# Optimization experiments

Hardware: AMD Instinct MI355X
Metric: run time of the kernel (lower is better)

Reference implementation:

```python
import jax, jax.numpy as jnp
import numpy as np

# Module constants (from init_kwargs)
NB_IN = 4          # num_blocks_in
NB_OUT = 8         # num_blocks_out
BS_IN = 128        # block_size_in (hard-coded in source)
NHID = 4096
BS_OUT = NHID // NB_OUT   # 512, also att_out
TOPK = 4
DK = 64            # d_k = d_v, n_head = 1


def _group_linear(x, w):
    # x: (B, n_blocks, d_in), w: (n_blocks, d_in, d_out) -> (B, n_blocks, d_out)
    return jnp.einsum('bnd,nde->bne', x, w)


def _attend(q, k, v):
    # single-head scaled dot-product attention
    attn = jax.nn.softmax(jnp.einsum('bqd,bkd->bqk', q, k) / jnp.sqrt(jnp.asarray(DK, q.dtype)), axis=-1)
    return jnp.einsum('bqk,bkd->bqd', attn, v), attn


def setup_inputs() -> dict:
    key = jax.random.key(0)
    ks = jax.random.split(key, 20)
    s = 0.02
    d = {
        'inp': jax.random.normal(ks[0], (1024, NB_IN * BS_IN), jnp.float32),
        'hx': jax.random.normal(ks[1], (1024, NHID), jnp.float32),
        'cx': jax.random.normal(ks[2], (1024, NHID), jnp.float32),
        # inp_att (residual=False): GroupLinear q/k/v + fc
        'ia_wq': jax.random.normal(ks[3], (NB_OUT, BS_OUT, DK), jnp.float32) * s,
        'ia_wk': jax.random.normal(ks[4], (NB_IN + 1, BS_IN, DK), jnp.float32) * s,
        'ia_wv': jax.random.normal(ks[5], (NB_IN + 1, BS_IN, DK), jnp.float32) * s,
        'ia_fc_w': jax.random.normal(ks[6], (DK, BS_OUT), jnp.float32) * s,
        'ia_fc_b': jnp.zeros((BS_OUT,), jnp.float32),
        # mha (residual=True, gated)
        'mha_wq': jax.random.normal(ks[7], (NB_OUT, BS_OUT, DK), jnp.float32) * s,
        'mha_wk': jax.random.normal(ks[8], (NB_OUT, BS_OUT, DK), jnp.float32) * s,
        'mha_wv': jax.random.normal(ks[9], (NB_OUT, BS_OUT, DK), jnp.float32) * s,
        'mha_fc_w': jax.random.normal(ks[10], (DK, BS_OUT), jnp.float32) * s,
        'mha_fc_b': jnp.zeros((BS_OUT,), jnp.float32),
        'mha_gate_w': jax.random.normal(ks[11], (DK, BS_OUT), jnp.float32) * s,
        'mha_gate_b': jnp.zeros((BS_OUT,), jnp.float32),
        # block-diagonal LSTM (BlockLSTM after blockify_params): per-block LSTMCell
        'w_ih': jax.random.normal(ks[12], (NB_OUT, BS_OUT, 4 * BS_OUT), jnp.float32) * s,
        'w_hh': jax.random.normal(ks[13], (NB_OUT, BS_OUT, 4 * BS_OUT), jnp.float32) * s,
        'b_ih': jnp.zeros((NB_OUT, 4 * BS_OUT), jnp.float32),
        'b_hh': jnp.zeros((NB_OUT, 4 * BS_OUT), jnp.float32),
    }
    return d


def _forward(inp, hx, cx, ia_wq, ia_wk, ia_wv, ia_fc_w, ia_fc_b,
             mha_wq, mha_wk, mha_wv, mha_fc_w, mha_fc_b, mha_gate_w, mha_gate_b,
             w_ih, w_hh, b_ih, b_hh):
    B = inp.shape[0]
    # --- input attention (inp_att) ---
    x = inp.reshape(B, NB_IN, BS_IN)
    x = jnp.concatenate([x, jnp.zeros_like(x[:, :1])], axis=1)        # append null block -> (B, NB_IN+1, BS_IN)
    hb = hx.reshape(B, NB_OUT, BS_OUT)
    q = _group_linear(hb, ia_wq)                                      # (B, NB_OUT, DK)
    k = _group_linear(x, ia_wk)
    v = _group_linear(x, ia_wv)
    o, iatt = _attend(q, k, v)                                        # o:(B,NB_OUT,DK), iatt:(B,NB_OUT,NB_IN+1)
    inp_use = (o @ ia_fc_w + ia_fc_b).reshape(B, NB_OUT * BS_OUT)     # residual=False path

    # --- top-k block selection mask (detached) ---
    score = iatt[:, :, 0]                                             # (B, NB_OUT)
    thr = jax.lax.top_k(score, TOPK)[0][:, -1]                        # k-th largest per sample
    mask_blk = (score > thr[:, None] - 0.01).astype(hx.dtype)         # (B, NB_OUT)
    mask = jnp.broadcast_to(mask_blk[:, :, None], (B, NB_OUT, BS_OUT)).reshape(B, NHID)
    mask = jax.lax.stop_gradient(mask)

    # --- block-diagonal LSTM update ---
    xb = inp_use.reshape(B, NB_OUT, BS_OUT)
    cb = cx.reshape(B, NB_OUT, BS_OUT)
    gates = (jnp.einsum('bkd,kdg->bkg', xb, w_ih) + b_ih
             + jnp.einsum('bkd,kdg->bkg', hb, w_hh) + b_hh)           # (B, NB_OUT, 4*BS_OUT)
    i_g, f_g, g_g, o_g = jnp.split(gates, 4, axis=-1)
    c_new = jax.nn.sigmoid(f_g) * cb + jax.nn.sigmoid(i_g) * jnp.tanh(g_g)
    h_new = jax.nn.sigmoid(o_g) * jnp.tanh(c_new)                     # (B, NB_OUT, BS_OUT)
    cx_new = c_new.reshape(B, NHID)

    # --- inter-block attention (step_att, residual + gate) ---
    residual = h_new
    q2 = _group_linear(h_new, mha_wq)
    k2 = _group_linear(h_new, mha_wk)
    v2 = _group_linear(h_new, mha_wv)
    o2, _ = _attend(q2, k2, v2)                                       # (B, NB_OUT, DK)
    out = o2 @ mha_fc_w + mha_fc_b
    gate = jax.nn.sigmoid(o2 @ mha_gate_w + mha_gate_b)
    hx_new = (residual + gate * jnp.tanh(out)).reshape(B, NHID)

    # --- masked blend of old / new states ---
    hx_out = mask * hx_new + (1.0 - mask) * hx
    cx_out = mask * cx_new + (1.0 - mask) * cx
    return hx_out, cx_out, mask


def reference(inp, hx, cx, ia_wq, ia_wk, ia_wv, ia_fc_w, ia_fc_b,
              mha_wq, mha_wk, mha_wv, mha_fc_w, mha_fc_b, mha_gate_w, mha_gate_b,
              w_ih, w_hh, b_ih, b_hh):
    return _forward(inp, hx, cx, ia_wq, ia_wk, ia_wv, ia_fc_w, ia_fc_b,
                    mha_wq, mha_wk, mha_wv, mha_fc_w, mha_fc_b, mha_gate_w, mha_gate_b,
                    w_ih, w_hh, b_ih, b_hh)
```

## Files before the change

kernel.cpp:

```cpp
#include <hip/hip_runtime.h>
#include <hip/hip_bf16.h>

#define B_    1024
#define NHID_ 4096
#define NBO   8
#define BSO   512
#define DK_   64

typedef __bf16 bf16;
typedef __bf16 bf16x2 __attribute__((ext_vector_type(2)));
typedef __bf16 bf16x4 __attribute__((ext_vector_type(4)));
typedef __bf16 bf16x8 __attribute__((ext_vector_type(8)));
typedef float  f32x4  __attribute__((ext_vector_type(4)));

__device__ __forceinline__ float sigf(float x){
    float e = __expf(-x);
    return __builtin_amdgcn_rcpf(1.0f + e);
}
__device__ __forceinline__ float ftanh(float x){
    float e = __expf(2.0f*x);
    return 1.0f - 2.0f*__builtin_amdgcn_rcpf(e + 1.0f);
}

__device__ __forceinline__ void gload16(const void* g, void* lds){
    __builtin_amdgcn_global_load_lds((const __attribute__((address_space(1))) unsigned int*)g,
                                     (__attribute__((address_space(3))) unsigned int*)lds,
                                     16, 0, 0);
}

__global__ __launch_bounds__(256) void k_prep(
    const float* __restrict__ w_ih, const float* __restrict__ w_hh,
    const float* __restrict__ hx,
    const float* __restrict__ mha_wq, const float* __restrict__ mha_wk,
    const float* __restrict__ mha_wv, const float* __restrict__ ia_fc_w,
    const float* __restrict__ fc_w, const float* __restrict__ gate_w,
    bf16* __restrict__ wT, bf16* __restrict__ hb16, bf16* __restrict__ wqkvT,
    bf16* __restrict__ iafcT, bf16* __restrict__ fcgT)
{
    int bid = blockIdx.x;
    int t = threadIdx.x;
    if (bid < 4096){
        int c0 = (bid & 31)*64;
        int k0 = ((bid>>5)&7)*64;
        int z  = bid>>8;
        int n = z>>1, which = z&1;
        const float* src = (which ? w_hh : w_ih) + (size_t)n*512*2048;
        __shared__ float tile[64][65];
        #pragma unroll
        for (int it=0; it<4; ++it){
            int idx = t + it*256;
            int r = idx>>4, c4 = (idx&15)*4;
            *(float4*)&tile[r][c4] = *(const float4*)&src[(size_t)(k0+r)*2048 + c0 + c4];
        }
        __syncthreads();
        #pragma unroll
        for (int it=0; it<2; ++it){
            int idx = t + it*256;
            int c = idx>>3, r8 = (idx&7)*8;
            bf16x8 v;
            #pragma unroll
            for (int jj=0;jj<8;++jj) v[jj] = (bf16)tile[r8+jj][c];
            *(bf16x8*)&wT[((size_t)n*2048 + c0 + c)*1024 + which*512 + k0 + r8] = v;
        }
        return;
    }
    int gid = (bid-4096)*256 + t;
    if (gid < 1048576){
        float4 v = ((const float4*)hx)[gid];
        bf16x4 o; o.x=(bf16)v.x; o.y=(bf16)v.y; o.z=(bf16)v.z; o.w=(bf16)v.w;
        *(bf16x4*)&hb16[(size_t)gid*4] = o;
        return;
    }
    int e = gid - 1048576;
    if (e < 786432){
        int col = e >> 9, k = e & 511;
        int n = col / 192, c = col - n*192;
        int p = c >> 6, ee = c & 63;
        const float* s = (p==0) ? mha_wq : ((p==1) ? mha_wk : mha_wv);
        wqkvT[e] = (bf16)s[((size_t)n*512 + k)*64 + ee];
        return;
    }
    e -= 786432;
    if (e < 32768){
        int c = e>>6, k = e&63;
        iafcT[e] = (bf16)ia_fc_w[(size_t)k*512 + c];
        return;
    }
    e -= 32768;
    if (e < 65536){
        int cg = e>>6, k = e&63;
        int ct = cg>>6, j = cg&63;
        const float* s = (j<32) ? fc_w : gate_w;
        int col = ct*32 + (j&31);
        fcgT[e] = (bf16)s[(size_t)k*512 + col];
    }
}

__global__ __launch_bounds__(256) void k_qkv(const float* __restrict__ hx,
                                             const float* __restrict__ inp,
                                             const float* __restrict__ ia_wq,
                                             const float* __restrict__ ia_wk,
                                             const float* __restrict__ ia_wv,
                                             float* __restrict__ qbuf,
                                             float* __restrict__ kbuf,
                                             float* __restrict__ vbuf)
{
    int b0 = blockIdx.x*32, y = blockIdx.y, t = threadIdx.x;
    int tx = t&15, ty = t>>4;
    __shared__ float Af[32][36];
    __shared__ float W1[32][68];
    __shared__ float W2[32][68];
    if (y < 8){
        int n = y;
        float acc[2][4] = {};
        for (int k0=0; k0<512; k0+=32){
            { int row=t>>3, c4=(t&7)*4;
              *(float4*)&Af[row][c4] = *(const float4*)&hx[(size_t)(b0+row)*4096 + n*512 + k0 + c4]; }
            #pragma unroll
            for (int j=0;j<2;++j){
                int id = j*256 + t;
                int kk = id>>4, e4 = (id&15)*4;
                *(float4*)&W1[kk][e4] = *(const float4*)&ia_wq[(size_t)n*32768 + (size_t)(k0+kk)*64 + e4];
            }
            __syncthreads();
            #pragma unroll
            for (int kk4=0; kk4<8; ++kk4){
                float4 a0 = *(float4*)&Af[ty*2  ][kk4*4];
                float4 a1 = *(float4*)&Af[ty*2+1][kk4*4];
                #pragma unroll
                for (int j=0;j<4;++j){
                    float4 wv = *(float4*)&W1[kk4*4+j][tx*4];
                    float s0 = (j==0)?a0.x:((j==1)?a0.y:((j==2)?a0.z:a0.w));
                    float s1 = (j==0)?a1.x:((j==1)?a1.y:((j==2)?a1.z:a1.w));
                    acc[0][0]+=s0*wv.x; acc[0][1]+=s0*wv.y; acc[0][2]+=s0*wv.z; acc[0][3]+=s0*wv.w;
                    acc[1][0]+=s1*wv.x; acc[1][1]+=s1*wv.y; acc[1][2]+=s1*wv.z; acc[1][3]+=s1*wv.w;
                }
            }
            __syncthreads();
        }
        #pragma unroll
        for (int r=0;r<2;++r){
            float4 o; o.x=acc[r][0]; o.y=acc[r][1]; o.z=acc[r][2]; o.w=acc[r][3];
            *(float4*)&qbuf[(size_t)(b0+ty*2+r)*512 + n*64 + tx*4] = o;
        }
    } else {
        int jb = y-8;
        float ak[2][4] = {}, av[2][4] = {};
        for (int k0=0; k0<128; k0+=32){
            { int row=t>>3, c4=(t&7)*4;
              *(float4*)&Af[row][c4] = *(const float4*)&inp[(size_t)(b0+row)*512 + jb*128 + k0 + c4]; }
            #pragma unroll
            for (int j=0;j<2;++j){
                int id = j*256 + t;
                int kk = id>>4, e4 = (id&15)*4;
                *(float4*)&W1[kk][e4] = *(const float4*)&ia_wk[(size_t)jb*8192 + (size_t)(k0+kk)*64 + e4];
                *(float4*)&W2[kk][e4] = *(const float4*)&ia_wv[(size_t)jb*8192 + (size_t)(k0+kk)*64 + e4];
            }
            __syncthreads();
            #pragma unroll
            for (int kk4=0; kk4<8; ++kk4){
                float4 a0 = *(float4*)&Af[ty*2  ][kk4*4];
                float4 a1 = *(float4*)&Af[ty*2+1][kk4*4];
                #pragma unroll
                for (int j=0;j<4;++j){
                    float4 wk = *(float4*)&W1[kk4*4+j][tx*4];
                    float4 wv = *(float4*)&W2[kk4*4+j][tx*4];
                    float s0 = (j==0)?a0.x:((j==1)?a0.y:((j==2)?a0.z:a0.w));
                    float s1 = (j==0)?a1.x:((j==1)?a1.y:((j==2)?a1.z:a1.w));
                    ak[0][0]+=s0*wk.x; ak[0][1]+=s0*wk.y; ak[0][2]+=s0*wk.z; ak[0][3]+=s0*wk.w;
                    ak[1][0]+=s1*wk.x; ak[1][1]+=s1*wk.y; ak[1][2]+=s1*wk.z; ak[1][3]+=s1*wk.w;
                    av[0][0]+=s0*wv.x; av[0][1]+=s0*wv.y; av[0][2]+=s0*wv.z; av[0][3]+=s0*wv.w;
                    av[1][0]+=s1*wv.x; av[1][1]+=s1*wv.y; av[1][2]+=s1*wv.z; av[1][3]+=s1*wv.w;
                }
            }
            __syncthreads();
        }
        #pragma unroll
        for (int r=0;r<2;++r){
            float4 ok; ok.x=ak[r][0]; ok.y=ak[r][1]; ok.z=ak[r][2]; ok.w=ak[r][3];
            float4 ov; ov.x=av[r][0]; ov.y=av[r][1]; ov.z=av[r][2]; ov.w=av[r][3];
            *(float4*)&kbuf[(size_t)(b0+ty*2+r)*256 + jb*64 + tx*4] = ok;
            *(float4*)&vbuf[(size_t)(b0+ty*2+r)*256 + jb*64 + tx*4] = ov;
        }
    }
}

__global__ __launch_bounds__(256) void k_score(const float* __restrict__ qbuf,
                                               const float* __restrict__ kbuf,
                                               const float* __restrict__ vbuf,
                                               bf16* __restrict__ obuf,
                                               float* __restrict__ maskb,
                                               float* __restrict__ mask_out)
{
    int t = threadIdx.x, sb = t>>6, ts = t&63;
    int b = blockIdx.x*4 + sb;
    __shared__ float q_s[4][512];
    __shared__ float k_s[4][256];
    __shared__ float v_s[4][256];
    __shared__ float at_s[4][40];
    __shared__ float sc_s[4][8];
    __shared__ float mb_s[4][8];

    #pragma unroll
    for (int r=0;r<8;++r) q_s[sb][ts+r*64] = qbuf[(size_t)b*512 + ts + r*64];
    #pragma unroll
    for (int r=0;r<4;++r){
        k_s[sb][ts+r*64] = kbuf[(size_t)b*256 + ts + r*64];
        v_s[sb][ts+r*64] = vbuf[(size_t)b*256 + ts + r*64];
    }
    __syncthreads();
    if (ts < 40){
        int n = ts/5, j = ts%5;
        float s = 0.f;
        if (j < 4){
            const float* q = &q_s[sb][n*64];
            const float* k = &k_s[sb][j*64];
            for (int e=0;e<64;++e) s += q[e]*k[e];
            s *= 0.125f;
        }
        at_s[sb][ts] = s;
    }
    __syncthreads();
    if (ts < 8){
        float m = at_s[sb][ts*5];
        for (int j=1;j<5;++j) m = fmaxf(m, at_s[sb][ts*5+j]);
        float ex[5]; float sum=0.f;
        for (int j=0;j<5;++j){ ex[j]=__expf(at_s[sb][ts*5+j]-m); sum+=ex[j]; }
        float inv = 1.f/sum;
        for (int j=0;j<5;++j) at_s[sb][ts*5+j] = ex[j]*inv;
        sc_s[sb][ts] = ex[0]*inv;
    }
    __syncthreads();
    if (ts == 0){
        float s[8];
        for (int nn=0;nn<8;++nn) s[nn] = sc_s[sb][nn];
        for (int ii=1;ii<8;++ii){ float key=s[ii]; int jj=ii-1;
            while(jj>=0 && s[jj]<key){ s[jj+1]=s[jj]; --jj; } s[jj+1]=key; }
        float thr = s[3]-0.01f;
        for (int nn=0;nn<8;++nn) mb_s[sb][nn] = (sc_s[sb][nn] > thr) ? 1.0f : 0.0f;
    }
    __syncthreads();
    #pragma unroll
    for (int r=0;r<8;++r){
        int i = ts + r*64;
        int n = i>>6, e = i&63;
        float s = 0.f;
        #pragma unroll
        for (int j=0;j<4;++j) s += at_s[sb][n*5+j]*v_s[sb][j*64+e];
        obuf[(size_t)b*512 + i] = (bf16)s;
    }
    if (ts < 8) maskb[b*8+ts] = mb_s[sb][ts];
    float4* mo = (float4*)(mask_out + (size_t)b*4096);
    #pragma unroll
    for (int r=0;r<16;++r){
        int i4 = ts + r*64;
        float m = mb_s[sb][i4>>7];
        float4 mv; mv.x=m; mv.y=m; mv.z=m; mv.w=m;
        mo[i4] = mv;
    }
}

__global__ __launch_bounds__(256) void k_fc_ia(const bf16* __restrict__ obuf,
                                               const bf16* __restrict__ iafcT,
                                               const float* __restrict__ ia_fc_b,
                                               bf16* __restrict__ xb16)
{
    int bx = blockIdx.x, by = blockIdx.y;
    int t = threadIdx.x, w = t>>6, l = t&63, quad = l>>4, l16 = l&15;
    int wm = w&1, wd = w>>1;
    __shared__ bf16 A_s[64*72];
    __shared__ bf16 W_s[64*72];
    #pragma unroll
    for (int j=0;j<2;++j){
        int c = t + j*256;
        int row = c>>3, seg = c&7;
        *(bf16x8*)&A_s[row*72 + seg*8] = *(const bf16x8*)&obuf[((size_t)bx*64+row)*64 + seg*8];
        *(bf16x8*)&W_s[row*72 + seg*8] = *(const bf16x8*)&iafcT[((size_t)by*64+row)*64 + seg*8];
    }
    __syncthreads();
    f32x4 zero = {0.f,0.f,0.f,0.f};
    f32x4 acc[2][2] = {{zero,zero},{zero,zero}};
    #pragma unroll
    for (int k0=0;k0<64;k0+=32){
        bf16x8 a[2], bb[2];
        #pragma unroll
        for (int r=0;r<2;++r) a[r] = *(const bf16x8*)&A_s[(wm*32+r*16+l16)*72 + k0 + quad*8];
        #pragma unroll
        for (int c=0;c<2;++c) bb[c] = *(const bf16x8*)&W_s[(wd*32+c*16+l16)*72 + k0 + quad*8];
        #pragma unroll
        for (int r=0;r<2;++r)
            #pragma unroll
            for (int c=0;c<2;++c)
                acc[r][c] = __builtin_amdgcn_mfma_f32_16x16x32_bf16(a[r], bb[c], acc[r][c], 0,0,0);
    }
    #pragma unroll
    for (int c=0;c<2;++c){
        int col = by*64 + wd*32 + c*16 + l16;
        float bias = ia_fc_b[col];
        #pragma unroll
        for (int r=0;r<2;++r)
            #pragma unroll
            for (int v=0;v<4;++v){
                int row = bx*64 + wm*32 + r*16 + quad*4 + v;
                xb16[(size_t)row*512 + col] = (bf16)(acc[r][c][v] + bias);
            }
    }
}

__global__ __launch_bounds__(256,4) void k_lstm(
    const bf16* __restrict__ xb16, const bf16* __restrict__ hb16,
    const bf16* __restrict__ wT, const float* __restrict__ b_ih,
    const float* __restrict__ b_hh, const float* __restrict__ cx,
    const float* __restrict__ maskb,
    float* __restrict__ cx_out, bf16* __restrict__ hn16)
{
    int bid = blockIdx.x;
    int n = bid & 7;
    int i = bid >> 3;
    int d0 = (i & 15) * 32;
    int b0 = (i >> 4) * 128;
    int t = threadIdx.x;
    int w = t >> 6, l = t & 63;
    int quad = l >> 4, l16 = l & 15;
    int wm = w & 1, wd = w >> 1;

    __shared__ bf16 A_s[2][512*8];
    __shared__ bf16 W_s[2][512*8];

    f32x4 zero = {0.f,0.f,0.f,0.f};
    f32x4 acc[4][4];
    #pragma unroll
    for (int rf=0;rf<4;++rf)
        #pragma unroll
        for (int g=0;g<4;++g) acc[rf][g] = zero;

    const bf16* wbase = wT + (size_t)n*2048*1024;

    auto stage = [&](int buf, int k0){
        const bf16* ab = (k0 < 512) ? (xb16 + (size_t)n*512 + k0)
                                    : (hb16 + (size_t)n*512 + (k0-512));
        #pragma unroll
        for (int j=0;j<2;++j){
            int slot = j*256 + w*64 + l;
            int row = slot>>2, ss = slot&3;
            int seg = ss ^ ((row>>1)&3);
            gload16(ab + (size_t)(b0+row)*4096 + seg*8, &A_s[buf][(j*256 + w*64)*8]);
        }
        #pragma unroll
        for (int j=0;j<2;++j){
            int slot = j*256 + w*64 + l;
            int col = slot>>2, ss = slot&3;
            int seg = ss ^ ((col>>1)&3);
            int g = col>>5, dl = col&31;
            gload16(wbase + (size_t)(g*512 + d0 + dl)*1024 + k0 + seg*8,
                    &W_s[buf][(j*256 + w*64)*8]);
        }
    };

    stage(0, 0);
    for (int it = 0; it < 32; ++it){
        __syncthreads();
        if (it < 31) stage((it+1)&1, (it+1)*32);
        int buf = it & 1;
        bf16x8 a[4];
        #pragma unroll
        for (int rf=0;rf<4;++rf){
            int row = wm*64 + rf*16 + l16;
            int slot = row*4 + (quad ^ ((row>>1)&3));
            a[rf] = *(const bf16x8*)&A_s[buf][slot*8];
        }
        #pragma unroll
        for (int g=0; g<4; ++g){
            int col = g*32 + wd*16 + l16;
            int slot = col*4 + (quad ^ ((col>>1)&3));
            bf16x8 bb = *(const bf16x8*)&W_s[buf][slot*8];
            #pragma unroll
            for (int rf=0;rf<4;++rf)
                acc[rf][g] = __builtin_amdgcn_mfma_f32_16x16x32_bf16(a[rf], bb, acc[rf][g], 0,0,0);
        }
    }

    int d = d0 + wd*16 + l16;
    float bi  = b_ih[n*2048 +        d] + b_hh[n*2048 +        d];
    float bff = b_ih[n*2048 +  512 + d] + b_hh[n*2048 +  512 + d];
    float bg  = b_ih[n*2048 + 1024 + d] + b_hh[n*2048 + 1024 + d];
    float bo  = b_ih[n*2048 + 1536 + d] + b_hh[n*2048 + 1536 + d];
    #pragma unroll
    for (int rf=0;rf<4;++rf){
        #pragma unroll
        for (int v=0;v<4;++v){
            int row = b0 + wm*64 + rf*16 + quad*4 + v;
            float gi = acc[rf][0][v] + bi;
            float gf = acc[rf][1][v] + bff;
            float gg = acc[rf][2][v] + bg;
            float go = acc[rf][3][v] + bo;
            size_t gidx = (size_t)row*4096 + n*512 + d;
            float cb = cx[gidx];
            float cn = sigf(gf)*cb + sigf(gi)*ftanh(gg);
            float hn = sigf(go)*ftanh(cn);
            float m  = maskb[row*8+n];
            cx_out[gidx] = (m != 0.f) ? cn : cb;
            hn16[gidx]   = (bf16)hn;
        }
    }
}

__global__ __launch_bounds__(256) void k_proj64(const bf16* __restrict__ hn16,
                                                const bf16* __restrict__ wqkvT,
                                                float* __restrict__ qkv2)
{
    int b0 = blockIdx.x*64, n = blockIdx.y, ct = blockIdx.z;
    int t = threadIdx.x, w = t>>6, l = t&63, quad = l>>4, l16 = l&15;
    int wm = w&1, wd = w>>1;
    __shared__ bf16 A_s[2][256*8];
    __shared__ bf16 B_s[2][256*8];
    f32x4 zero = {0.f,0.f,0.f,0.f};
    f32x4 acc[2][2] = {{zero,zero},{zero,zero}};
    const bf16* ab = hn16 + (size_t)n*512;
    const bf16* wb = wqkvT + ((size_t)n*192 + ct*64)*512;

    auto stage = [&](int buf, int k0){
        int row = t>>2, ss = t&3;
        int seg = ss ^ ((row>>1)&3);
        gload16(ab + (size_t)(b0+row)*4096 + k0 + seg*8, &A_s[buf][(w*64)*8]);
        gload16(wb + (size_t)row*512      + k0 + seg*8, &B_s[buf][(w*64)*8]);
    };

    stage(0, 0);
    for (int it=0; it<16; ++it){
        __syncthreads();
        if (it < 15) stage((it+1)&1, (it+1)*32);
        int buf = it&1;
        bf16x8 a[2], bb[2];
        #pragma unroll
        for (int r=0;r<2;++r){
            int row = wm*32 + r*16 + l16;
            int slot = row*4 + (quad ^ ((row>>1)&3));
            a[r] = *(const bf16x8*)&A_s[buf][slot*8];
        }
        #pragma unroll
        for (int c=0;c<2;++c){
            int col = wd*32 + c*16 + l16;
            int slot = col*4 + (quad ^ ((col>>1)&3));
            bb[c] = *(const bf16x8*)&B_s[buf][slot*8];
        }
        #pragma unroll
        for (int r=0;r<2;++r)
            #pragma unroll
            for (int c=0;c<2;++c)
                acc[r][c] = __builtin_amdgcn_mfma_f32_16x16x32_bf16(a[r], bb[c], acc[r][c], 0,0,0);
    }
    #pragma unroll
    for (int c=0;c<2;++c){
        int col = ct*64 + wd*32 + c*16 + l16;
        #pragma unroll
        for (int r=0;r<2;++r)
            #pragma unroll
            for (int v=0;v<4;++v){
                int row = b0 + wm*32 + r*16 + quad*4 + v;
                qkv2[(size_t)row*1536 + n*192 + col] = acc[r][c][v];
            }
    }
}

__global__ __launch_bounds__(256) void k_att2(const float* __restrict__ qkv2,
                                              bf16* __restrict__ o2buf)
{
    int t = threadIdx.x, sb = t>>6, ts = t&63;
    int b = blockIdx.x*4 + sb;
    __shared__ float q_s[4][512];
    __shared__ float k_s[4][512];
    __shared__ float v_s[4][512];
    __shared__ float at_s[4][64];
    #pragma unroll
    for (int r=0;r<8;++r){
        int i = ts + r*64;
        int n = i>>6, e = i&63;
        const float* src = qkv2 + (size_t)b*1536 + n*192;
        q_s[sb][i] = src[e];
        k_s[sb][i] = src[64+e];
        v_s[sb][i] = src[128+e];
    }
    __syncthreads();
    {
        int n = ts>>3, j = ts&7;
        float s = 0.f;
        const float* q = &q_s[sb][n*64];
        const float* k = &k_s[sb][j*64];
        for (int e=0;e<64;++e) s += q[e]*k[e];
        at_s[sb][ts] = s*0.125f;
    }
    __syncthreads();
    if (ts < 8){
        float m = at_s[sb][ts*8];
        for (int j=1;j<8;++j) m = fmaxf(m, at_s[sb][ts*8+j]);
        float ex[8]; float sum=0.f;
        for (int j=0;j<8;++j){ ex[j]=__expf(at_s[sb][ts*8+j]-m); sum+=ex[j]; }
        float inv = 1.f/sum;
        for (int j=0;j<8;++j) at_s[sb][ts*8+j] = ex[j]*inv;
    }
    __syncthreads();
    #pragma unroll
    for (int r=0;r<8;++r){
        int i = ts + r*64;
        int n = i>>6, e = i&63;
        float s = 0.f;
        #pragma unroll
        for (int j=0;j<8;++j) s += at_s[sb][n*8+j]*v_s[sb][j*64+e];
        o2buf[(size_t)b*512 + i] = (bf16)s;
    }
}

__global__ __launch_bounds__(256) void k_fcgate(const bf16* __restrict__ o2buf,
                                                const bf16* __restrict__ fcgT,
                                                const float* __restrict__ fc_b,
                                                const float* __restrict__ gate_b,
                                                const bf16* __restrict__ hn16,
                                                const float* __restrict__ hx,
                                                const float* __restrict__ maskb,
                                                float* __restrict__ hx_out)
{
    int bx = blockIdx.x, ct0 = blockIdx.y*2;
    int t = threadIdx.x, w = t>>6, l = t&63, quad = l>>4, l16 = l&15;
    __shared__ bf16 A_s[64*72];
    __shared__ bf16 W_s[2][64*72];
    #pragma unroll
    for (int j=0;j<2;++j){
        int c = t + j*256;
        int row = c>>3, seg = c&7;
        *(bf16x8*)&A_s[row*72 + seg*8] = *(const bf16x8*)&o2buf[((size_t)bx*64+row)*64 + seg*8];
        *(bf16x8*)&W_s[0][row*72 + seg*8] = *(const bf16x8*)&fcgT[((size_t)ct0*64+row)*64 + seg*8];
        *(bf16x8*)&W_s[1][row*72 + seg*8] = *(const bf16x8*)&fcgT[((size_t)(ct0+1)*64+row)*64 + seg*8];
    }
    __syncthreads();
    f32x4 zero = {0.f,0.f,0.f,0.f};
    #pragma unroll
    for (int cc=0; cc<2; ++cc){
        int ct = ct0 + cc;
        f32x4 acc[4] = {zero,zero,zero,zero};
        #pragma unroll
        for (int k0=0;k0<64;k0+=32){
            bf16x8 a = *(const bf16x8*)&A_s[(w*16+l16)*72 + k0 + quad*8];
            #pragma unroll
            for (int c=0;c<4;++c){
                bf16x8 bb = *(const bf16x8*)&W_s[cc][(c*16+l16)*72 + k0 + quad*8];
                acc[c] = __builtin_amdgcn_mfma_f32_16x16x32_bf16(a, bb, acc[c], 0,0,0);
            }
        }
        #pragma unroll
        for (int c=0;c<2;++c){
            int d = ct*32 + c*16 + l16;
            float fb = fc_b[d], gb = gate_b[d];
            #pragma unroll
            for (int v=0;v<4;++v){
                int row = bx*64 + w*16 + quad*4 + v;
                int b = row>>3, n = row&7;
                size_t idx = (size_t)b*4096 + n*512 + d;
                float f = acc[c][v]   + fb;
                float g = acc[c+2][v] + gb;
                float hn = (float)hn16[idx];
                float m = maskb[row];
                hx_out[idx] = (m != 0.f) ? (hn + sigf(g)*ftanh(f)) : hx[idx];
            }
        }
    }
}

extern "C" void kernel_launch(void* const* d_in, const int* in_sizes, int n_in,
                              void* d_out, int out_size, void* d_ws, size_t ws_size,
                              hipStream_t stream)
{
    const float* inp       = (const float*)d_in[0];
    const float* hx        = (const float*)d_in[1];
    const float* cx        = (const float*)d_in[2];
    const float* ia_wq     = (const float*)d_in[3];
    const float* ia_wk     = (const float*)d_in[4];
    const float* ia_wv     = (const float*)d_in[5];
    const float* ia_fc_w   = (const float*)d_in[6];
    const float* ia_fc_b   = (const float*)d_in[7];
    const float* mha_wq    = (const float*)d_in[8];
    const float* mha_wk    = (const float*)d_in[9];
    const float* mha_wv    = (const float*)d_in[10];
    const float* mha_fc_w  = (const float*)d_in[11];
    const float* mha_fc_b  = (const float*)d_in[12];
    const float* mha_gate_w= (const float*)d_in[13];
    const float* mha_gate_b= (const float*)d_in[14];
    const float* w_ih      = (const float*)d_in[15];
    const float* w_hh      = (const float*)d_in[16];
    const float* b_ih      = (const float*)d_in[17];
    const float* b_hh      = (const float*)d_in[18];

    float* hx_out  = (float*)d_out;
    float* cx_out  = hx_out + (size_t)B_*NHID_;
    float* mask_out= cx_out + (size_t)B_*NHID_;

    char* p = (char*)d_ws;
    bf16* wT     = (bf16*)p;               p += (size_t)8*2048*1024*2;
    bf16* hb16   = (bf16*)p;               p += (size_t)B_*NHID_*2;
    bf16* xb16   = (bf16*)p;               p += (size_t)B_*NHID_*2;
    bf16* hn16   = (bf16*)p;               p += (size_t)B_*NHID_*2;
    bf16* wqkvT  = (bf16*)p;               p += (size_t)8*192*512*2;
    bf16* iafcT  = (bf16*)p;               p += (size_t)512*64*2;
    bf16* fcgT   = (bf16*)p;               p += (size_t)1024*64*2;
    float* qbuf  = (float*)p;              p += (size_t)B_*512*4;
    float* kbuf  = (float*)p;              p += (size_t)B_*256*4;
    float* vbuf  = (float*)p;              p += (size_t)B_*256*4;
    bf16* obuf   = (bf16*)p;               p += (size_t)B_*8*64*2;
    bf16* o2buf  = (bf16*)p;               p += (size_t)B_*8*64*2;
    float* qkv2  = (float*)p;              p += (size_t)B_*1536*4;
    float* maskb = (float*)p;              p += (size_t)B_*8*4;

    hipLaunchKernelGGL(k_prep, dim3(11648), dim3(256), 0, stream,
                       w_ih, w_hh, hx, mha_wq, mha_wk, mha_wv, ia_fc_w, mha_fc_w, mha_gate_w,
                       wT, hb16, wqkvT, iafcT, fcgT);
    hipLaunchKernelGGL(k_qkv, dim3(32,12), dim3(256), 0, stream,
                       hx, inp, ia_wq, ia_wk, ia_wv, qbuf, kbuf, vbuf);
    hipLaunchKernelGGL(k_score, dim3(256), dim3(256), 0, stream,
                       qbuf, kbuf, vbuf, obuf, maskb, mask_out);
    hipLaunchKernelGGL(k_fc_ia, dim3(128,8), dim3(256), 0, stream, obuf, iafcT, ia_fc_b, xb16);
    hipLaunchKernelGGL(k_lstm, dim3(1024), dim3(256), 0, stream,
                       xb16, hb16, wT, b_ih, b_hh, cx, maskb, cx_out, hn16);
    hipLaunchKernelGGL(k_proj64, dim3(16,8,3), dim3(256), 0, stream, hn16, wqkvT, qkv2);
    hipLaunchKernelGGL(k_att2, dim3(256), dim3(256), 0, stream, qkv2, o2buf);
    hipLaunchKernelGGL(k_fcgate, dim3(128,8), dim3(256), 0, stream,
                       o2buf, fcgT, mha_fc_b, mha_gate_b, hn16, hx, maskb, hx_out);
}
```

Before: 291.1 us.

## Retile LSTM GEMM to 256x256 tiles with 4-stage LDS pipeline

Rewrites the block-diagonal LSTM GEMM kernel to use 512-thread workgroups computing 256x256 output tiles (256 workgroups instead of 1024), with a four-buffer LDS ring, split A/B prefetch phases, manual vmcnt waits and raw barriers, and setprio around MFMA bursts. The epilogue is staged through LDS so each thread handles one hidden column across all four gates, which gives coalesced cx/cx_out/hn16 accesses. The aim is more operand reuse per loaded byte and better overlap of loads with MFMA work. The cost is higher register and LDS pressure and only 256 workgroups, which may underfill the 256 CUs.

```diff
diff --git a/kernel.cpp b/kernel.cpp
--- a/kernel.cpp
+++ b/kernel.cpp
@@ -27,6 +27,13 @@
                                      (__attribute__((address_space(3))) unsigned int*)lds,
                                      16, 0, 0);
 }
+
+__device__ __forceinline__ void sbar(){
+    asm volatile("" ::: "memory");
+    __builtin_amdgcn_s_barrier();
+    asm volatile("" ::: "memory");
+}
+#define WAITVM(N) asm volatile("s_waitcnt vmcnt(" #N ")" ::: "memory")
 
 __global__ __launch_bounds__(256) void k_prep(
     const float* __restrict__ w_ih, const float* __restrict__ w_hh,
@@ -307,7 +314,7 @@
     }
 }
 
-__global__ __launch_bounds__(256,4) void k_lstm(
+__global__ __launch_bounds__(512,2) void k_lstm(
     const bf16* __restrict__ xb16, const bf16* __restrict__ hb16,
     const bf16* __restrict__ wT, const float* __restrict__ b_ih,
     const float* __restrict__ b_hh, const float* __restrict__ cx,
@@ -315,93 +322,139 @@
     float* __restrict__ cx_out, bf16* __restrict__ hn16)
 {
     int bid = blockIdx.x;
-    int n = bid & 7;
-    int i = bid >> 3;
-    int d0 = (i & 15) * 32;
-    int b0 = (i >> 4) * 128;
+    int n  = bid & 7;
+    int i  = bid >> 3;
+    int mt = i & 3, nt = i >> 2;
+    int b0 = mt*256, d0 = nt*64;
+
     int t = threadIdx.x;
     int w = t >> 6, l = t & 63;
+    int wr = w >> 2, wc = w & 3;
     int quad = l >> 4, l16 = l & 15;
-    int wm = w & 1, wd = w >> 1;
-
-    __shared__ bf16 A_s[2][512*8];
-    __shared__ bf16 W_s[2][512*8];
+
+    __shared__ __align__(16) bf16 lds[4*16384];
+
+    int G0 = t;
+    int rowA0 = G0>>2, rowA1 = rowA0 + 128;
+    int ksA0 = (G0&3) ^ ((rowA0>>1)&3);
+    int ksA1 = (G0&3) ^ ((rowA1>>1)&3);
+    const bf16* xbP0 = xb16 + (size_t)(b0+rowA0)*4096 + n*512 + ksA0*8;
+    const bf16* hbP0 = hb16 + (size_t)(b0+rowA0)*4096 + n*512 + ksA0*8;
+    const bf16* xbP1 = xb16 + (size_t)(b0+rowA1)*4096 + n*512 + ksA1*8;
+    const bf16* hbP1 = hb16 + (size_t)(b0+rowA1)*4096 + n*512 + ksA1*8;
+
+    int vc0 = G0>>2, vc1 = vc0 + 128;
+    int ksB0 = (G0&3) ^ ((vc0>>1)&3);
+    int ksB1 = (G0&3) ^ ((vc1>>1)&3);
+    const bf16* wb = wT + (size_t)n*2048*1024;
+    const bf16* wP0 = wb + (size_t)((vc0>>6)*512 + d0 + (vc0&63))*1024 + ksB0*8;
+    const bf16* wP1 = wb + (size_t)((vc1>>6)*512 + d0 + (vc1&63))*1024 + ksB1*8;
+
+    int offA[8], offB[4];
+    #pragma unroll
+    for (int m=0;m<8;++m){ int R = wr*128 + m*16 + l16; offA[m] = (R*4 + (quad ^ ((R>>1)&3)))*8; }
+    #pragma unroll
+    for (int nf=0;nf<4;++nf){ int C = wc*64 + nf*16 + l16; offB[nf] = (C*4 + (quad ^ ((C>>1)&3)))*8; }
+
+    auto stA = [&](int buf, int kt){
+        const bf16* s0 = (kt<16 ? xbP0 : hbP0) + (kt&15)*32;
+        const bf16* s1 = (kt<16 ? xbP1 : hbP1) + (kt&15)*32;
+        bf16* dst = &lds[buf*16384 + w*512];
+        gload16(s0, dst);
+        gload16(s1, dst + 4096);
+    };
+    auto stB = [&](int buf, int kt){
+        bf16* dst = &lds[buf*16384 + 8192 + w*512];
+        gload16(wP0 + kt*32, dst);
+        gload16(wP1 + kt*32, dst + 4096);
+    };
 
     f32x4 zero = {0.f,0.f,0.f,0.f};
-    f32x4 acc[4][4];
-    #pragma unroll
-    for (int rf=0;rf<4;++rf)
-        #pragma unroll
-        for (int g=0;g<4;++g) acc[rf][g] = zero;
-
-    const bf16* wbase = wT + (size_t)n*2048*1024;
-
-    auto stage = [&](int buf, int k0){
-        const bf16* ab = (k0 < 512) ? (xb16 + (size_t)n*512 + k0)
-                                    : (hb16 + (size_t)n*512 + (k0-512));
-        #pragma unroll
-        for (int j=0;j<2;++j){
-            int slot = j*256 + w*64 + l;
-            int row = slot>>2, ss = slot&3;
-            int seg = ss ^ ((row>>1)&3);
-            gload16(ab + (size_t)(b0+row)*4096 + seg*8, &A_s[buf][(j*256 + w*64)*8]);
-        }
-        #pragma unroll
-        for (int j=0;j<2;++j){
-            int slot = j*256 + w*64 + l;
-            int col = slot>>2, ss = slot&3;
-            int seg = ss ^ ((col>>1)&3);
-            int g = col>>5, dl = col&31;
-            gload16(wbase + (size_t)(g*512 + d0 + dl)*1024 + k0 + seg*8,
-                    &W_s[buf][(j*256 + w*64)*8]);
-        }
-    };
-
-    stage(0, 0);
-    for (int it = 0; it < 32; ++it){
-        __syncthreads();
-        if (it < 31) stage((it+1)&1, (it+1)*32);
-        int buf = it & 1;
-        bf16x8 a[4];
-        #pragma unroll
-        for (int rf=0;rf<4;++rf){
-            int row = wm*64 + rf*16 + l16;
-            int slot = row*4 + (quad ^ ((row>>1)&3));
-            a[rf] = *(const bf16x8*)&A_s[buf][slot*8];
-        }
-        #pragma unroll
-        for (int g=0; g<4; ++g){
-            int col = g*32 + wd*16 + l16;
-            int slot = col*4 + (quad ^ ((col>>1)&3));
-            bf16x8 bb = *(const bf16x8*)&W_s[buf][slot*8];
-            #pragma unroll
-            for (int rf=0;rf<4;++rf)
-                acc[rf][g] = __builtin_amdgcn_mfma_f32_16x16x32_bf16(a[rf], bb, acc[rf][g], 0,0,0);
-        }
-    }
-
-    int d = d0 + wd*16 + l16;
+    f32x4 acc[8][4];
+    #pragma unroll
+    for (int m=0;m<8;++m)
+        #pragma unroll
+        for (int nf=0;nf<4;++nf) acc[m][nf] = zero;
+
+    stA(0,0); stB(0,0);
+    stA(1,1); stB(1,1);
+    WAITVM(4);
+    sbar();
+
+    #pragma unroll 2
+    for (int kt=0; kt<32; ++kt){
+        int buf = kt & 3;
+        const bf16* Ab = &lds[buf*16384];
+        const bf16* Bb = Ab + 8192;
+        bf16x8 av[4], bv[4];
+
+        if (kt < 30) stA((kt+2)&3, kt+2);
+        #pragma unroll
+        for (int m=0;m<4;++m) av[m] = *(const bf16x8*)&Ab[offA[m]];
+        #pragma unroll
+        for (int nf=0;nf<4;++nf) bv[nf] = *(const bf16x8*)&Bb[offB[nf]];
+        __builtin_amdgcn_s_setprio(1);
+        #pragma unroll
+        for (int m=0;m<4;++m)
+            #pragma unroll
+            for (int nf=0;nf<4;++nf)
+                acc[m][nf] = __builtin_amdgcn_mfma_f32_16x16x32_bf16(av[m], bv[nf], acc[m][nf], 0,0,0);
+        __builtin_amdgcn_s_setprio(0);
+        sbar();
+
+        if (kt < 30) stB((kt+2)&3, kt+2);
+        #pragma unroll
+        for (int m=0;m<4;++m) av[m] = *(const bf16x8*)&Ab[offA[4+m]];
+        __builtin_amdgcn_s_setprio(1);
+        #pragma unroll
+        for (int m=0;m<4;++m)
+            #pragma unroll
+            for (int nf=0;nf<4;++nf)
+                acc[4+m][nf] = __builtin_amdgcn_mfma_f32_16x16x32_bf16(av[m], bv[nf], acc[4+m][nf], 0,0,0);
+        __builtin_amdgcn_s_setprio(0);
+        if (kt < 30) { WAITVM(4); } else { WAITVM(0); }
+        sbar();
+    }
+
+    float* gbuf = (float*)lds;
+    const int GP = 260;
+    int dl_t = t & 63;
+    int i_t  = t >> 6;
+    int d = d0 + dl_t;
     float bi  = b_ih[n*2048 +        d] + b_hh[n*2048 +        d];
     float bff = b_ih[n*2048 +  512 + d] + b_hh[n*2048 +  512 + d];
     float bg  = b_ih[n*2048 + 1024 + d] + b_hh[n*2048 + 1024 + d];
     float bo  = b_ih[n*2048 + 1536 + d] + b_hh[n*2048 + 1536 + d];
-    #pragma unroll
-    for (int rf=0;rf<4;++rf){
-        #pragma unroll
-        for (int v=0;v<4;++v){
-            int row = b0 + wm*64 + rf*16 + quad*4 + v;
-            float gi = acc[rf][0][v] + bi;
-            float gf = acc[rf][1][v] + bff;
-            float gg = acc[rf][2][v] + bg;
-            float go = acc[rf][3][v] + bo;
-            size_t gidx = (size_t)row*4096 + n*512 + d;
+
+    #pragma unroll
+    for (int c=0; c<4; ++c){
+        if (wr == (c>>1)){
+            #pragma unroll
+            for (int mm=0; mm<4; ++mm)
+                #pragma unroll
+                for (int nf=0; nf<4; ++nf)
+                    #pragma unroll
+                    for (int v=0; v<4; ++v)
+                        gbuf[(mm*16 + quad*4 + v)*GP + wc*64 + nf*16 + l16] = acc[(c&1)*4 + mm][nf][v];
+        }
+        __syncthreads();
+        #pragma unroll
+        for (int r=0; r<8; ++r){
+            int row_l = i_t*8 + r;
+            int row_g = b0 + c*64 + row_l;
+            float gi = gbuf[row_l*GP +       dl_t] + bi;
+            float gf = gbuf[row_l*GP +  64 + dl_t] + bff;
+            float gg = gbuf[row_l*GP + 128 + dl_t] + bg;
+            float go = gbuf[row_l*GP + 192 + dl_t] + bo;
+            size_t gidx = (size_t)row_g*4096 + n*512 + d;
             float cb = cx[gidx];
             float cn = sigf(gf)*cb + sigf(gi)*ftanh(gg);
             float hn = sigf(go)*ftanh(cn);
-            float m  = maskb[row*8+n];
-            cx_out[gidx] = (m != 0.f) ? cn : cb;
+            float mk = maskb[row_g*8 + n];
+            cx_out[gidx] = (mk != 0.f) ? cn : cb;
             hn16[gidx]   = (bf16)hn;
         }
+        __syncthreads();
     }
 }
 
@@ -618,7 +671,7 @@
     hipLaunchKernelGGL(k_score, dim3(256), dim3(256), 0, stream,
                        qbuf, kbuf, vbuf, obuf, maskb, mask_out);
     hipLaunchKernelGGL(k_fc_ia, dim3(128,8), dim3(256), 0, stream, obuf, iafcT, ia_fc_b, xb16);
-    hipLaunchKernelGGL(k_lstm, dim3(1024), dim3(256), 0, stream,
+    hipLaunchKernelGGL(k_lstm, dim3(256), dim3(512), 0, stream,
                        xb16, hb16, wT, b_ih, b_hh, cx, maskb, cx_out, hn16);
     hipLaunchKernelGGL(k_proj64, dim3(16,8,3), dim3(256), 0, stream, hn16, wqkvT, qkv2);
     hipLaunchKernelGGL(k_att2, dim3(256), dim3(256), 0, stream, qkv2, o2buf);
```

After: 285.7 us. Within noise of the previous version (-1.8%).
